# Optimization experiments

Measured on AMD Instinct MI355X. Metric: run time of the kernel, lower is better.

Reference implementation:

```python
import jax, jax.numpy as jnp
import numpy as np

B, P, ENC_DIM = 256, 196, 2048
WORD_DIM, ATT_DIM = 512, 512

def setup_inputs() -> dict:
    key = jax.random.key(0)
    ks = jax.random.split(key, 8)
    s_enc = 1.0 / np.sqrt(ENC_DIM)
    s_dec = 1.0 / np.sqrt(WORD_DIM)
    s_fin = 1.0 / np.sqrt(ATT_DIM)
    return {
        "encoder_out": jax.random.normal(ks[0], (B, P, ENC_DIM), dtype=jnp.float32),
        "decoder_out": jax.random.normal(ks[1], (B, WORD_DIM), dtype=jnp.float32),
        "W_enc": jax.random.uniform(ks[2], (ENC_DIM, ATT_DIM), jnp.float32, -s_enc, s_enc),
        "b_enc": jax.random.uniform(ks[3], (ATT_DIM,), jnp.float32, -s_enc, s_enc),
        "W_dec": jax.random.uniform(ks[4], (WORD_DIM, ATT_DIM), jnp.float32, -s_dec, s_dec),
        "b_dec": jax.random.uniform(ks[5], (ATT_DIM,), jnp.float32, -s_dec, s_dec),
        "W_fin": jax.random.uniform(ks[6], (ATT_DIM,), jnp.float32, -s_fin, s_fin),
        "b_fin": jax.random.uniform(ks[7], (), jnp.float32, -s_fin, s_fin),
    }

def reference(encoder_out, decoder_out, W_enc, b_enc, W_dec, b_dec, W_fin, b_fin):
    # encoder projection: [B, P, A]
    att_enc = jnp.einsum('bpe,ea->bpa', encoder_out, W_enc) + b_enc
    # decoder projection: [B, A]
    att_dec = decoder_out @ W_dec + b_dec
    # additive combine + relu + final scalar projection -> [B, P]
    hidden = jax.nn.relu(att_enc + att_dec[:, None, :])
    att = jnp.einsum('bpa,a->bp', hidden, W_fin) + b_fin
    # softmax over pixels (dim=1)
    att_weights = jax.nn.softmax(att, axis=1)
    # weighted sum of encoder features -> [B, ENC_DIM]
    return jnp.einsum('bpe,bp->be', encoder_out, att_weights)
```

## Files before the change

kernel.cpp:

```cpp
#include <hip/hip_runtime.h>

#define B_   256
#define P_   196
#define E_   2048
#define WD_  512
#define A_   512
#define M_   (B_ * P_)

typedef __bf16 bf16x8 __attribute__((ext_vector_type(8)));
typedef float  f32x4  __attribute__((ext_vector_type(4)));

using u16 = unsigned short;
using u32 = unsigned int;

__device__ inline u16 f2bf(float f) {
    u32 u; __builtin_memcpy(&u, &f, 4);
    u32 lsb = (u >> 16) & 1u; u += 0x7FFFu + lsb; return (u16)(u >> 16);
}

__device__ inline void gload_lds16(const void* g, void* lds) {
    __builtin_amdgcn_global_load_lds(
        (const __attribute__((address_space(1))) u32*)g,
        (__attribute__((address_space(3))) u32*)lds, 16, 0, 0);
}

__global__ __launch_bounds__(256) void k_prep(const float* __restrict__ We,
                                              u16* __restrict__ Wt) {
    __shared__ float tile[32][33];
    const int tx = threadIdx.x & 31, ty = threadIdx.x >> 5;
    const int k0 = blockIdx.x * 32, n0 = blockIdx.y * 32;
#pragma unroll
    for (int i = 0; i < 4; ++i)
        tile[ty + i * 8][tx] = We[(size_t)(k0 + ty + i * 8) * A_ + n0 + tx];
    __syncthreads();
#pragma unroll
    for (int i = 0; i < 4; ++i)
        Wt[(size_t)(n0 + ty + i * 8) * E_ + k0 + tx] = f2bf(tile[tx][ty + i * 8]);
}

__global__ __launch_bounds__(512) void k_att_dec(const float* __restrict__ dec,
                                                 const float* __restrict__ Wd,
                                                 const float* __restrict__ bd,
                                                 float* __restrict__ att_dec) {
    int b = blockIdx.x, a = threadIdx.x;
    __shared__ float sd[WD_];
    sd[a] = dec[b * WD_ + a];
    __syncthreads();
    float acc = bd[a];
#pragma unroll 8
    for (int e = 0; e < WD_; ++e)
        acc = fmaf(sd[e], Wd[e * A_ + a], acc);
    att_dec[b * A_ + a] = acc;
}

__global__ __launch_bounds__(256, 2) void k_logits(
        const float* __restrict__ enc, const u16* __restrict__ Wt,
        const float* __restrict__ be, const float* __restrict__ Wf,
        const float* __restrict__ att_dec, float* __restrict__ att) {
    __shared__ bf16x8 sA[4 * 2 * 64];
    __shared__ bf16x8 sB[32 * 2 * 64];
    __shared__ float  sred[4][64];

    const int t   = threadIdx.x;
    const int w   = t >> 6;
    const int L   = t & 63;
    const int l15 = L & 15;
    const int q   = L >> 4;
    const int m0  = blockIdx.x * 64;

    const f32x4 zero = {0.f, 0.f, 0.f, 0.f};
    f32x4 acc[4][8];
#pragma unroll
    for (int rt = 0; rt < 4; ++rt)
#pragma unroll
        for (int ct = 0; ct < 8; ++ct) acc[rt][ct] = zero;

    const float* ag = enc + (size_t)(m0 + w * 16 + l15) * E_ + q * 8;
    const u16*   bg = Wt + (size_t)(w * 8 * 16 + l15) * E_ + q * 8;

    for (int k0 = 0; k0 < E_; k0 += 64) {
#pragma unroll
        for (int s = 0; s < 2; ++s) {
            const float* ap = ag + k0 + s * 32;
            float4 f0 = *(const float4*)(ap);
            float4 f1 = *(const float4*)(ap + 4);
            u16 h[8];
            h[0] = f2bf(f0.x); h[1] = f2bf(f0.y); h[2] = f2bf(f0.z); h[3] = f2bf(f0.w);
            h[4] = f2bf(f1.x); h[5] = f2bf(f1.y); h[6] = f2bf(f1.z); h[7] = f2bf(f1.w);
            bf16x8 v; __builtin_memcpy(&v, h, 16);
            sA[(w * 2 + s) * 64 + L] = v;
        }
#pragma unroll
        for (int i = 0; i < 16; ++i) {
            int ctl = i >> 1, s = i & 1;
            const u16* gp = bg + (size_t)ctl * 16 * E_ + k0 + s * 32;
            gload_lds16(gp, (void*)&sB[((w * 8 + ctl) * 2 + s) * 64]);
        }
        __syncthreads();

#pragma unroll
        for (int s = 0; s < 2; ++s) {
            bf16x8 af[4], bfr[8];
#pragma unroll
            for (int rt = 0; rt < 4; ++rt) af[rt] = sA[(rt * 2 + s) * 64 + L];
#pragma unroll
            for (int ct = 0; ct < 8; ++ct) bfr[ct] = sB[((w * 8 + ct) * 2 + s) * 64 + L];
#pragma unroll
            for (int ct = 0; ct < 8; ++ct)
#pragma unroll
                for (int rt = 0; rt < 4; ++rt)
                    acc[rt][ct] = __builtin_amdgcn_mfma_f32_16x16x32_bf16(
                        af[rt], bfr[ct], acc[rt][ct], 0, 0, 0);
        }
        __syncthreads();
    }

    float wf[8], bev[8];
#pragma unroll
    for (int ct = 0; ct < 8; ++ct) {
        int n = w * 128 + ct * 16 + l15;
        wf[ct]  = Wf[n];
        bev[ct] = be[n];
    }
#pragma unroll
    for (int rt = 0; rt < 4; ++rt) {
#pragma unroll
        for (int reg = 0; reg < 4; ++reg) {
            int ml = rt * 16 + q * 4 + reg;
            int b  = (m0 + ml) / P_;
            const float* adp = att_dec + (size_t)b * A_ + w * 128 + l15;
            float p = 0.f;
#pragma unroll
            for (int ct = 0; ct < 8; ++ct) {
                float h = acc[rt][ct][reg] + bev[ct] + adp[ct * 16];
                p = fmaf(fmaxf(h, 0.f), wf[ct], p);
            }
#pragma unroll
            for (int off = 8; off > 0; off >>= 1)
                p += __shfl_down(p, off, 16);
            if (l15 == 0) sred[w][ml] = p;
        }
    }
    __syncthreads();
    if (t < 64)
        att[m0 + t] = sred[0][t] + sred[1][t] + sred[2][t] + sred[3][t];
}

__global__ __launch_bounds__(256) void k_out(const float* __restrict__ enc,
                                             const float* __restrict__ att,
                                             float* __restrict__ out) {
    int b = blockIdx.x, t = threadIdx.x;
    __shared__ float sw[P_];
    __shared__ float red[8];

    float v = (t < P_) ? att[b * P_ + t] : -1e30f;
    float m = v;
#pragma unroll
    for (int off = 32; off > 0; off >>= 1)
        m = fmaxf(m, __shfl_down(m, off, 64));
    int wid = t >> 6;
    if ((t & 63) == 0) red[wid] = m;
    __syncthreads();
    m = fmaxf(fmaxf(red[0], red[1]), fmaxf(red[2], red[3]));

    float ev = (t < P_) ? __expf(v - m) : 0.f;
    float s = ev;
#pragma unroll
    for (int off = 32; off > 0; off >>= 1)
        s += __shfl_down(s, off, 64);
    if ((t & 63) == 0) red[4 + wid] = s;
    __syncthreads();
    s = red[4] + red[5] + red[6] + red[7];
    if (t < P_) sw[t] = ev / s;
    __syncthreads();

    const int e0 = blockIdx.y * 1024 + t * 4;
    const float* ep = enc + (size_t)b * P_ * E_ + e0;
    f32x4 acc = {0.f, 0.f, 0.f, 0.f};
#pragma unroll 4
    for (int p = 0; p < P_; ++p) {
        float4 qv = *(const float4*)(ep + (size_t)p * E_);
        float wgt = sw[p];
        acc[0] = fmaf(wgt, qv.x, acc[0]);
        acc[1] = fmaf(wgt, qv.y, acc[1]);
        acc[2] = fmaf(wgt, qv.z, acc[2]);
        acc[3] = fmaf(wgt, qv.w, acc[3]);
    }
    float* op = out + (size_t)b * E_ + e0;
    op[0] = acc[0]; op[1] = acc[1]; op[2] = acc[2]; op[3] = acc[3];
}

extern "C" void kernel_launch(void* const* d_in, const int* in_sizes, int n_in,
                              void* d_out, int out_size, void* d_ws, size_t ws_size,
                              hipStream_t stream) {
    const float* enc   = (const float*)d_in[0];
    const float* dec   = (const float*)d_in[1];
    const float* W_enc = (const float*)d_in[2];
    const float* b_enc = (const float*)d_in[3];
    const float* W_dec = (const float*)d_in[4];
    const float* b_dec = (const float*)d_in[5];
    const float* W_fin = (const float*)d_in[6];

    float* att_dec = (float*)d_ws;
    float* att     = att_dec + B_ * A_;
    u16*   Wt      = (u16*)(att + M_);

    k_prep<<<dim3(E_ / 32, A_ / 32), 256, 0, stream>>>(W_enc, Wt);
    k_att_dec<<<B_, 512, 0, stream>>>(dec, W_dec, b_dec, att_dec);
    k_logits<<<M_ / 64, 256, 0, stream>>>(enc, Wt, b_enc, W_fin, att_dec, att);
    k_out<<<dim3(B_, 2), 256, 0, stream>>>(enc, att, (float*)d_out);
}
```

Measured before the change: 893.6 us.

## Pipeline logits GEMM with register-prefetched weights and split pixel reduction in output

Measured after the change: 870.4 us. 2.6% less time.

```diff
diff --git a/kernel.cpp b/kernel.cpp
--- a/kernel.cpp
+++ b/kernel.cpp
@@ -15,13 +15,7 @@
 
 __device__ inline u16 f2bf(float f) {
     u32 u; __builtin_memcpy(&u, &f, 4);
-    u32 lsb = (u >> 16) & 1u; u += 0x7FFFu + lsb; return (u16)(u >> 16);
-}
-
-__device__ inline void gload_lds16(const void* g, void* lds) {
-    __builtin_amdgcn_global_load_lds(
-        (const __attribute__((address_space(1))) u32*)g,
-        (__attribute__((address_space(3))) u32*)lds, 16, 0, 0);
+    u += 0x7FFFu + ((u >> 16) & 1u); return (u16)(u >> 16);
 }
 
 __global__ __launch_bounds__(256) void k_prep(const float* __restrict__ We,
@@ -53,13 +47,12 @@
     att_dec[b * A_ + a] = acc;
 }
 
-__global__ __launch_bounds__(256, 2) void k_logits(
+__global__ __launch_bounds__(512, 2) void k_logits(
         const float* __restrict__ enc, const u16* __restrict__ Wt,
         const float* __restrict__ be, const float* __restrict__ Wf,
         const float* __restrict__ att_dec, float* __restrict__ att) {
-    __shared__ bf16x8 sA[4 * 2 * 64];
-    __shared__ bf16x8 sB[32 * 2 * 64];
-    __shared__ float  sred[4][64];
+    __shared__ bf16x8 sA[2][256];
+    __shared__ float  sred[8][64];
 
     const int t   = threadIdx.x;
     const int w   = t >> 6;
@@ -69,56 +62,75 @@
     const int m0  = blockIdx.x * 64;
 
     const f32x4 zero = {0.f, 0.f, 0.f, 0.f};
-    f32x4 acc[4][8];
+    f32x4 acc[4][4];
 #pragma unroll
     for (int rt = 0; rt < 4; ++rt)
 #pragma unroll
-        for (int ct = 0; ct < 8; ++ct) acc[rt][ct] = zero;
-
-    const float* ag = enc + (size_t)(m0 + w * 16 + l15) * E_ + q * 8;
-    const u16*   bg = Wt + (size_t)(w * 8 * 16 + l15) * E_ + q * 8;
-
-    for (int k0 = 0; k0 < E_; k0 += 64) {
-#pragma unroll
-        for (int s = 0; s < 2; ++s) {
-            const float* ap = ag + k0 + s * 32;
-            float4 f0 = *(const float4*)(ap);
-            float4 f1 = *(const float4*)(ap + 4);
-            u16 h[8];
-            h[0] = f2bf(f0.x); h[1] = f2bf(f0.y); h[2] = f2bf(f0.z); h[3] = f2bf(f0.w);
-            h[4] = f2bf(f1.x); h[5] = f2bf(f1.y); h[6] = f2bf(f1.z); h[7] = f2bf(f1.w);
-            bf16x8 v; __builtin_memcpy(&v, h, 16);
-            sA[(w * 2 + s) * 64 + L] = v;
-        }
-#pragma unroll
-        for (int i = 0; i < 16; ++i) {
-            int ctl = i >> 1, s = i & 1;
-            const u16* gp = bg + (size_t)ctl * 16 * E_ + k0 + s * 32;
-            gload_lds16(gp, (void*)&sB[((w * 8 + ctl) * 2 + s) * 64]);
-        }
+        for (int ct = 0; ct < 4; ++ct) acc[rt][ct] = zero;
+
+    const int s    = t >> 1, h = t & 1;
+    const int srt  = s >> 6;
+    const int sL   = s & 63;
+    const float* ap = enc + (size_t)(m0 + srt * 16 + (sL & 15)) * E_
+                          + (sL >> 4) * 8 + h * 4;
+    u32* slds = (u32*)&sA[0][s] + h * 2;
+    u32* slds1 = (u32*)&sA[1][s] + h * 2;
+
+    const u16* bp = Wt + (size_t)(w * 64 + l15) * E_ + q * 8;
+    const size_t bstep = (size_t)16 * E_;
+
+    uint4 bcur[4], bnxt[4];
+#pragma unroll
+    for (int ct = 0; ct < 4; ++ct)
+        bcur[ct] = *(const uint4*)(bp + ct * bstep);
+    float4 aN1 = *(const float4*)(ap);
+    float4 aN2 = *(const float4*)(ap + 32);
+    {
+        u32 lo = (u32)f2bf(aN1.x) | ((u32)f2bf(aN1.y) << 16);
+        u32 hi = (u32)f2bf(aN1.z) | ((u32)f2bf(aN1.w) << 16);
+        slds[0] = lo; slds[1] = hi;
+    }
+    aN1 = aN2;
+    __syncthreads();
+
+    for (int k = 0; k < 64; ++k) {
+        const int buf = k & 1;
+        bf16x8 af[4];
+#pragma unroll
+        for (int rt = 0; rt < 4; ++rt) af[rt] = sA[buf][rt * 64 + L];
+
+        const int kA = (k + 2 < 64) ? k + 2 : 63;
+        const int kB = (k + 1 < 64) ? k + 1 : 63;
+        aN2 = *(const float4*)(ap + (size_t)kA * 32);
+#pragma unroll
+        for (int ct = 0; ct < 4; ++ct)
+            bnxt[ct] = *(const uint4*)(bp + ct * bstep + (size_t)kB * 32);
+
+#pragma unroll
+        for (int ct = 0; ct < 4; ++ct) {
+            bf16x8 bv; __builtin_memcpy(&bv, &bcur[ct], 16);
+#pragma unroll
+            for (int rt = 0; rt < 4; ++rt)
+                acc[rt][ct] = __builtin_amdgcn_mfma_f32_16x16x32_bf16(
+                    af[rt], bv, acc[rt][ct], 0, 0, 0);
+        }
+
+        {
+            u32 lo = (u32)f2bf(aN1.x) | ((u32)f2bf(aN1.y) << 16);
+            u32 hi = (u32)f2bf(aN1.z) | ((u32)f2bf(aN1.w) << 16);
+            u32* d = buf ? slds : slds1;
+            d[0] = lo; d[1] = hi;
+        }
+        aN1 = aN2;
+#pragma unroll
+        for (int ct = 0; ct < 4; ++ct) bcur[ct] = bnxt[ct];
         __syncthreads();
-
-#pragma unroll
-        for (int s = 0; s < 2; ++s) {
-            bf16x8 af[4], bfr[8];
-#pragma unroll
-            for (int rt = 0; rt < 4; ++rt) af[rt] = sA[(rt * 2 + s) * 64 + L];
-#pragma unroll
-            for (int ct = 0; ct < 8; ++ct) bfr[ct] = sB[((w * 8 + ct) * 2 + s) * 64 + L];
-#pragma unroll
-            for (int ct = 0; ct < 8; ++ct)
-#pragma unroll
-                for (int rt = 0; rt < 4; ++rt)
-                    acc[rt][ct] = __builtin_amdgcn_mfma_f32_16x16x32_bf16(
-                        af[rt], bfr[ct], acc[rt][ct], 0, 0, 0);
-        }
-        __syncthreads();
-    }
-
-    float wf[8], bev[8];
-#pragma unroll
-    for (int ct = 0; ct < 8; ++ct) {
-        int n = w * 128 + ct * 16 + l15;
+    }
+
+    float wf[4], bev[4];
+#pragma unroll
+    for (int ct = 0; ct < 4; ++ct) {
+        int n = w * 64 + ct * 16 + l15;
         wf[ct]  = Wf[n];
         bev[ct] = be[n];
     }
@@ -128,12 +140,12 @@
         for (int reg = 0; reg < 4; ++reg) {
             int ml = rt * 16 + q * 4 + reg;
             int b  = (m0 + ml) / P_;
-            const float* adp = att_dec + (size_t)b * A_ + w * 128 + l15;
+            const float* adp = att_dec + (size_t)b * A_ + w * 64 + l15;
             float p = 0.f;
 #pragma unroll
-            for (int ct = 0; ct < 8; ++ct) {
-                float h = acc[rt][ct][reg] + bev[ct] + adp[ct * 16];
-                p = fmaf(fmaxf(h, 0.f), wf[ct], p);
+            for (int ct = 0; ct < 4; ++ct) {
+                float hx = acc[rt][ct][reg] + bev[ct] + adp[ct * 16];
+                p = fmaf(fmaxf(hx, 0.f), wf[ct], p);
             }
 #pragma unroll
             for (int off = 8; off > 0; off >>= 1)
@@ -142,8 +154,12 @@
         }
     }
     __syncthreads();
-    if (t < 64)
-        att[m0 + t] = sred[0][t] + sred[1][t] + sred[2][t] + sred[3][t];
+    if (t < 64) {
+        float r = 0.f;
+#pragma unroll
+        for (int ww = 0; ww < 8; ++ww) r += sred[ww][t];
+        att[m0 + t] = r;
+    }
 }
 
 __global__ __launch_bounds__(256) void k_out(const float* __restrict__ enc,
@@ -152,6 +168,7 @@
     int b = blockIdx.x, t = threadIdx.x;
     __shared__ float sw[P_];
     __shared__ float red[8];
+    __shared__ f32x4 spart[4][64];
 
     float v = (t < P_) ? att[b * P_ + t] : -1e30f;
     float m = v;
@@ -164,21 +181,24 @@
     m = fmaxf(fmaxf(red[0], red[1]), fmaxf(red[2], red[3]));
 
     float ev = (t < P_) ? __expf(v - m) : 0.f;
-    float s = ev;
+    float ssum = ev;
 #pragma unroll
     for (int off = 32; off > 0; off >>= 1)
-        s += __shfl_down(s, off, 64);
-    if ((t & 63) == 0) red[4 + wid] = s;
-    __syncthreads();
-    s = red[4] + red[5] + red[6] + red[7];
-    if (t < P_) sw[t] = ev / s;
-    __syncthreads();
-
-    const int e0 = blockIdx.y * 1024 + t * 4;
+        ssum += __shfl_down(ssum, off, 64);
+    if ((t & 63) == 0) red[4 + wid] = ssum;
+    __syncthreads();
+    ssum = red[4] + red[5] + red[6] + red[7];
+    if (t < P_) sw[t] = ev / ssum;
+    __syncthreads();
+
+    const int tq = t >> 6, lane = t & 63;
+    const int e0 = blockIdx.y * 256 + lane * 4;
     const float* ep = enc + (size_t)b * P_ * E_ + e0;
     f32x4 acc = {0.f, 0.f, 0.f, 0.f};
-#pragma unroll 4
-    for (int p = 0; p < P_; ++p) {
+    const int p0 = tq * 49;
+#pragma unroll 7
+    for (int i = 0; i < 49; ++i) {
+        int p = p0 + i;
         float4 qv = *(const float4*)(ep + (size_t)p * E_);
         float wgt = sw[p];
         acc[0] = fmaf(wgt, qv.x, acc[0]);
@@ -186,8 +206,18 @@
         acc[2] = fmaf(wgt, qv.z, acc[2]);
         acc[3] = fmaf(wgt, qv.w, acc[3]);
     }
-    float* op = out + (size_t)b * E_ + e0;
-    op[0] = acc[0]; op[1] = acc[1]; op[2] = acc[2]; op[3] = acc[3];
+    spart[tq][lane] = acc;
+    __syncthreads();
+    if (tq == 0) {
+        f32x4 r = spart[0][lane];
+#pragma unroll
+        for (int g = 1; g < 4; ++g) {
+            f32x4 x = spart[g][lane];
+            r[0] += x[0]; r[1] += x[1]; r[2] += x[2]; r[3] += x[3];
+        }
+        float* op = out + (size_t)b * E_ + e0;
+        op[0] = r[0]; op[1] = r[1]; op[2] = r[2]; op[3] = r[3];
+    }
 }
 
 extern "C" void kernel_launch(void* const* d_in, const int* in_sizes, int n_in,
@@ -207,6 +237,6 @@
 
     k_prep<<<dim3(E_ / 32, A_ / 32), 256, 0, stream>>>(W_enc, Wt);
     k_att_dec<<<B_, 512, 0, stream>>>(dec, W_dec, b_dec, att_dec);
-    k_logits<<<M_ / 64, 256, 0, stream>>>(enc, Wt, b_enc, W_fin, att_dec, att);
-    k_out<<<dim3(B_, 2), 256, 0, stream>>>(enc, att, (float*)d_out);
-}
+    k_logits<<<M_ / 64, 512, 0, stream>>>(enc, Wt, b_enc, W_fin, att_dec, att);
+    k_out<<<dim3(B_, 8), 256, 0, stream>>>(enc, att, (float*)d_out);
+}
```
